# Kernel optimization log

Hardware: AMD Instinct MI355X
Metric: run time of the kernel (lower is better)

Reference implementation:

```python
import jax, jax.numpy as jnp
import numpy as np

HIDDEN = 1000
DICT = 4811
T = 44
B = 256


def _lstm_cell(x, h, c, W_ih, W_hh, b_ih, b_hh):
    # gates: [B, 4*H], PyTorch order i, f, g, o
    gates = x @ W_ih.T + b_ih + h @ W_hh.T + b_hh
    i, f, g, o = jnp.split(gates, 4, axis=-1)
    i = jax.nn.sigmoid(i)
    f = jax.nn.sigmoid(f)
    g = jnp.tanh(g)
    o = jax.nn.sigmoid(o)
    c_new = f * c + i * g
    h_new = o * jnp.tanh(c_new)
    return h_new, c_new


def setup_inputs() -> dict:
    key = jax.random.key(0)
    ks = jax.random.split(key, 20)
    s = 0.02
    H = HIDDEN
    return {
        "x": jax.random.normal(ks[0], (B, T, H), jnp.float32),
        "h1": jax.random.normal(ks[1], (B, H), jnp.float32),
        "h2": jax.random.normal(ks[2], (B, H), jnp.float32),
        "c1": jax.random.normal(ks[3], (B, H), jnp.float32),
        "c2": jax.random.normal(ks[4], (B, H), jnp.float32),
        "layer_W": jax.random.normal(ks[5], (H, H), jnp.float32) * s,
        "layer_b": jnp.zeros((H,), jnp.float32),
        "W_ih1": jax.random.normal(ks[6], (4 * H, 2 * H), jnp.float32) * s,
        "W_hh1": jax.random.normal(ks[7], (4 * H, H), jnp.float32) * s,
        "b_ih1": jnp.zeros((4 * H,), jnp.float32),
        "b_hh1": jnp.zeros((4 * H,), jnp.float32),
        "W_ih2": jax.random.normal(ks[8], (4 * H, DICT + 2 * H), jnp.float32) * s,
        "W_hh2": jax.random.normal(ks[9], (4 * H, H), jnp.float32) * s,
        "b_ih2": jnp.zeros((4 * H,), jnp.float32),
        "b_hh2": jnp.zeros((4 * H,), jnp.float32),
        "out_W": jax.random.normal(ks[10], (DICT, H), jnp.float32) * s,
        "out_b": jnp.zeros((DICT,), jnp.float32),
    }


def reference(x, h1, h2, c1, c2, layer_W, layer_b,
              W_ih1, W_hh1, b_ih1, b_hh1,
              W_ih2, W_hh2, b_ih2, b_hh2,
              out_W, out_b):
    # input projection: [B, T, H]
    xp = x @ layer_W.T + layer_b
    prev0 = jnp.zeros((x.shape[0], DICT), x.dtype)

    def step(carry, xt):
        h1, c1, h2, c2, prev = carry
        l1_in = jnp.concatenate([xt, h1], axis=1)            # [B, 2H]
        h1n, c1n = _lstm_cell(l1_in, h1, c1, W_ih1, W_hh1, b_ih1, b_hh1)
        l2_in = jnp.concatenate([prev, h2, h1n], axis=1)     # [B, DICT+2H]
        h2n, c2n = _lstm_cell(l2_in, h2, c2, W_ih2, W_hh2, b_ih2, b_hh2)
        logits = h2n @ out_W.T + out_b                       # [B, DICT]
        # NOTE: original torch code softmaxes over dim=0 (batch axis)
        y = jax.nn.softmax(logits, axis=0)
        return (h1n, c1n, h2n, c2n, y), y

    xs = jnp.transpose(xp, (1, 0, 2))                        # [T, B, H]
    _, ys = jax.lax.scan(step, (h1, c1, h2, c2, prev0), xs)
    return jnp.transpose(ys, (1, 0, 2))                      # [B, T, DICT]
```

## Files before the change

kernel.cpp:

```cpp
#include <hip/hip_runtime.h>
#include <hip/hip_bf16.h>

#define HID   1000
#define DICT  4811
#define TT    44
#define BB    256
#define G4    4000
#define G4P   4096
#define K1P   2048
#define K2P   6912
#define HP    1024
#define DP    4864
#define Z2_H2 4864
#define Z2_H1 5888
#define PD    3
#define GPART ((long long)BB * G4P)

typedef __attribute__((ext_vector_type(8))) short short8;
typedef __attribute__((ext_vector_type(4))) float f32x4;

__device__ __forceinline__ short f2b(float f) {
    unsigned u = __float_as_uint(f);
    unsigned r = (u + 0x7FFFu + ((u >> 16) & 1u)) >> 16;
    return (short)r;
}

__device__ __forceinline__ void gload16(const void* g, const short* l) {
    __builtin_amdgcn_global_load_lds(
        (const __attribute__((address_space(1))) unsigned int*)g,
        (__attribute__((address_space(3))) unsigned int*)l, 16, 0, 0);
}

__global__ void prep_w1p(const float* __restrict__ wih1, const float* __restrict__ whh1,
                         short* __restrict__ w) {
    for (size_t i = (size_t)blockIdx.x * blockDim.x + threadIdx.x; i < (size_t)G4P * K1P;
         i += (size_t)gridDim.x * blockDim.x) {
        int n = (int)(i >> 11), j = (int)(i & 2047);
        float v = 0.f;
        if (n < G4) {
            if (j < HID) v = wih1[(size_t)n * 2000 + j];
            else if (j >= 1024 && j < 1024 + HID) {
                int jj = j - 1024;
                v = wih1[(size_t)n * 2000 + HID + jj] + whh1[(size_t)n * HID + jj];
            }
        }
        w[i] = f2b(v);
    }
}

__global__ void prep_w2p(const float* __restrict__ wih2, const float* __restrict__ whh2,
                         short* __restrict__ w) {
    int n = blockIdx.y;
    int j = blockIdx.x * 256 + threadIdx.x;
    float v = 0.f;
    if (n < G4) {
        if (j < DICT) v = wih2[(size_t)n * 6811 + j];
        else if (j >= Z2_H2 && j < Z2_H2 + HID) {
            int jj = j - Z2_H2;
            v = wih2[(size_t)n * 6811 + DICT + jj] + whh2[(size_t)n * HID + jj];
        } else if (j >= Z2_H1 && j < Z2_H1 + HID) {
            int jj = j - Z2_H1;
            v = wih2[(size_t)n * 6811 + DICT + HID + jj];
        }
    }
    w[(size_t)n * K2P + j] = f2b(v);
}

__global__ void prep_outwp(const float* __restrict__ outw, short* __restrict__ w) {
    int n = blockIdx.y;
    int j = blockIdx.x * 256 + threadIdx.x;
    float v = (n < DICT && j < HID) ? outw[(size_t)n * HID + j] : 0.f;
    w[(size_t)n * HP + j] = f2b(v);
}

__global__ void prep_cvt(const float* __restrict__ src, short* __restrict__ dst, size_t n) {
    for (size_t i = (size_t)blockIdx.x * blockDim.x + threadIdx.x; i < n;
         i += (size_t)gridDim.x * blockDim.x)
        dst[i] = f2b(src[i]);
}

__global__ void prep_addv(const float* __restrict__ a, const float* __restrict__ b,
                          float* __restrict__ dst, int n) {
    int i = blockIdx.x * blockDim.x + threadIdx.x;
    if (i < n) dst[i] = a[i] + b[i];
}

__global__ void init_vec(const float* __restrict__ src, short* __restrict__ dst, int ld) {
    int i = blockIdx.x * blockDim.x + threadIdx.x;
    if (i >= BB * HID) return;
    int b = i / HID, h = i % HID;
    dst[(size_t)b * ld + h] = f2b(src[i]);
}

template <int EPI, int AF32>
__global__ __launch_bounds__(256) void gemm_nt(
    const void* __restrict__ Ap, int lda,
    const short* __restrict__ Bp, int ldb,
    const float* __restrict__ bias,
    void* __restrict__ Cp, long long partStride, int ldc,
    int M, int N, int Kvalid)
{
    __shared__ short As[64][40];
    __shared__ short Bs[64][40];
    const int tid  = threadIdx.x;
    const int lane = tid & 63;
    const int wave = tid >> 6;
    const int wm = wave >> 1, wn = wave & 1;
    const int tm = blockIdx.y * 64, tn = blockIdx.x * 64;
    const int srow = tid >> 2;
    const int scol = (tid & 3) * 8;

    const int nk = (Kvalid + 31) >> 5;
    const int s0 = (int)(((long long)nk * blockIdx.z) / gridDim.z);
    const int s1 = (int)(((long long)nk * (blockIdx.z + 1)) / gridDim.z);

    const int arow = tm + srow;
    const int brow = tn + srow;
    const bool bvalid = brow < N;

    auto loadA = [&](int ks) -> short8 {
        int k = (ks << 5) + scol;
        short8 r = {0, 0, 0, 0, 0, 0, 0, 0};
        if (k + 8 <= Kvalid) {
            if (AF32) {
                const f32x4* p = (const f32x4*)((const float*)Ap + (size_t)arow * lda + k);
                f32x4 u0 = p[0], u1 = p[1];
                r[0] = f2b(u0[0]); r[1] = f2b(u0[1]); r[2] = f2b(u0[2]); r[3] = f2b(u0[3]);
                r[4] = f2b(u1[0]); r[5] = f2b(u1[1]); r[6] = f2b(u1[2]); r[7] = f2b(u1[3]);
            } else {
                r = *(const short8*)((const short*)Ap + (size_t)arow * lda + k);
            }
        }
        return r;
    };
    auto loadB = [&](int ks) -> short8 {
        int k = (ks << 5) + scol;
        short8 r = {0, 0, 0, 0, 0, 0, 0, 0};
        if (bvalid && (k + 8 <= Kvalid))
            r = *(const short8*)(Bp + (size_t)brow * ldb + k);
        return r;
    };

    f32x4 acc[2][2];
    for (int a = 0; a < 2; ++a)
        for (int b = 0; b < 2; ++b)
            acc[a][b] = (f32x4){0.f, 0.f, 0.f, 0.f};

    short8 ra = loadA(s0), rb = loadB(s0);
    *(short8*)&As[srow][scol] = ra;
    *(short8*)&Bs[srow][scol] = rb;
    __syncthreads();

    const int kg = (lane >> 4) * 8;
    const int fr = lane & 15;

    for (int s = s0; s < s1; ++s) {
        short8 a0 = *(short8*)&As[wm * 32 + fr][kg];
        short8 a1 = *(short8*)&As[wm * 32 + 16 + fr][kg];
        short8 b0 = *(short8*)&Bs[wn * 32 + fr][kg];
        short8 b1 = *(short8*)&Bs[wn * 32 + 16 + fr][kg];
        short8 na, nb;
        if (s + 1 < s1) { na = loadA(s + 1); nb = loadB(s + 1); }
        acc[0][0] = __builtin_amdgcn_mfma_f32_16x16x32_bf16(a0, b0, acc[0][0], 0, 0, 0);
        acc[0][1] = __builtin_amdgcn_mfma_f32_16x16x32_bf16(a0, b1, acc[0][1], 0, 0, 0);
        acc[1][0] = __builtin_amdgcn_mfma_f32_16x16x32_bf16(a1, b0, acc[1][0], 0, 0, 0);
        acc[1][1] = __builtin_amdgcn_mfma_f32_16x16x32_bf16(a1, b1, acc[1][1], 0, 0, 0);
        __syncthreads();
        if (s + 1 < s1) {
            *(short8*)&As[srow][scol] = na;
            *(short8*)&Bs[srow][scol] = nb;
        }
        __syncthreads();
    }

    float* Cf = (float*)Cp + (size_t)partStride * blockIdx.z;
    for (int mi = 0; mi < 2; ++mi)
        for (int ni = 0; ni < 2; ++ni) {
            int col = tn + wn * 32 + ni * 16 + (lane & 15);
            if (col >= N) continue;
            float bv = bias ? bias[col] : 0.f;
            int row0 = tm + wm * 32 + mi * 16 + ((lane >> 4) << 2);
            f32x4 v = acc[mi][ni];
            for (int j = 0; j < 4; ++j) {
                int row = row0 + j;
                float val = v[j] + bv;
                if (EPI == 0) {
                    Cf[(size_t)row * ldc + col] = val;
                } else {
                    int b = row / TT, t = row % TT;
                    ((short*)Cp)[((size_t)t * BB + b) * ldc + col] = f2b(val);
                }
            }
        }
}

__global__ __launch_bounds__(512, 4) void gemm_s128(
    const short* __restrict__ A0, const short* __restrict__ A1, int splitA, int lda,
    const short* __restrict__ Bw, int ldb,
    float* __restrict__ C, long long partStride, int ldc, int nk)
{
    __shared__ __align__(16) short smem[PD][8192];
    const int tid  = threadIdx.x;
    const int lane = tid & 63;
    const int w    = tid >> 6;
    const int wm = w >> 2, wn = w & 3;
    const int tm = blockIdx.y * 128;
    const int tn = blockIdx.x * 128;
    const int s0 = (int)(((long long)nk * blockIdx.z) / gridDim.z);
    const int s1 = (int)(((long long)nk * (blockIdx.z + 1)) / gridDim.z);

    const int rA = tid >> 2, slA = tid & 3;
    const int swz = (slA ^ ((rA >> 1) & 3)) << 3;
    const size_t aoff = (size_t)(tm + rA) * lda + (size_t)swz;
    const size_t boff = (size_t)(tn + rA) * ldb + (size_t)swz;

    auto stage = [&](int buf, int s) {
        const int k0 = s << 5;
        const short* As = (k0 < splitA) ? A0 : A1;
        const short* l = &smem[buf][0];
        gload16(As + k0 + aoff, l + tid * 8);
        gload16(Bw + k0 + boff, l + 4096 + tid * 8);
    };

    const int fr = lane & 15;
    const int kg = lane >> 4;
    int aRd[4], bRd[2];
    #pragma unroll
    for (int mi = 0; mi < 4; ++mi) {
        int row = wm * 64 + mi * 16 + fr;
        aRd[mi] = row * 32 + ((kg ^ ((row >> 1) & 3)) << 3);
    }
    #pragma unroll
    for (int ni = 0; ni < 2; ++ni) {
        int row = wn * 32 + ni * 16 + fr;
        bRd[ni] = 4096 + row * 32 + ((kg ^ ((row >> 1) & 3)) << 3);
    }

    f32x4 acc[4][2];
    #pragma unroll
    for (int a = 0; a < 4; ++a)
        #pragma unroll
        for (int b = 0; b < 2; ++b)
            acc[a][b] = (f32x4){0.f, 0.f, 0.f, 0.f};

    #pragma unroll
    for (int i = 0; i < PD; ++i)
        if (s0 + i < s1) stage(i, s0 + i);

    int buf = 0;
    for (int s = s0; s < s1; ++s) {
        const int ahead = s1 - 1 - s;
        if (ahead >= 2)      asm volatile("s_waitcnt vmcnt(4)" ::: "memory");
        else if (ahead == 1) asm volatile("s_waitcnt vmcnt(2)" ::: "memory");
        else                 asm volatile("s_waitcnt vmcnt(0)" ::: "memory");
        __builtin_amdgcn_s_barrier();

        const short* bp = &smem[buf][0];
        short8 af[4], bf[2];
        #pragma unroll
        for (int i = 0; i < 4; ++i) af[i] = *(const short8*)(bp + aRd[i]);
        #pragma unroll
        for (int i = 0; i < 2; ++i) bf[i] = *(const short8*)(bp + bRd[i]);
        asm volatile("s_waitcnt lgkmcnt(0)" ::: "memory");
        __builtin_amdgcn_sched_barrier(0);
        __builtin_amdgcn_s_barrier();
        if (s + PD < s1) stage(buf, s + PD);

        #pragma unroll
        for (int mi = 0; mi < 4; ++mi)
            #pragma unroll
            for (int ni = 0; ni < 2; ++ni)
                acc[mi][ni] = __builtin_amdgcn_mfma_f32_16x16x32_bf16(af[mi], bf[ni], acc[mi][ni], 0, 0, 0);

        buf = (buf + 1 == PD) ? 0 : buf + 1;
    }

    float* Cp = C + (size_t)partStride * blockIdx.z;
    const int colb = tn + wn * 32 + fr;
    const int rowb = tm + wm * 64 + (kg << 2);
    #pragma unroll
    for (int mi = 0; mi < 4; ++mi)
        #pragma unroll
        for (int ni = 0; ni < 2; ++ni) {
            int col = colb + ni * 16;
            int row0 = rowb + mi * 16;
            #pragma unroll
            for (int j = 0; j < 4; ++j)
                Cp[(size_t)(row0 + j) * ldc + col] = acc[mi][ni][j];
        }
}

__global__ __launch_bounds__(512) void logits_sm(
    const short* __restrict__ A , const short* __restrict__ Bw ,
    const float* __restrict__ outb, float* __restrict__ out,
    short* __restrict__ z2, int t)
{
    __shared__ __align__(16) short smem[PD][10240];
    __shared__ float red[256];
    const int tid  = threadIdx.x;
    const int lane = tid & 63;
    const int w    = tid >> 6;
    const int wm = w >> 1, wn = w & 1;
    const int tn = blockIdx.x * 64;
    const int nk = HP / 32;

    const int cA0 = w * 64 + lane;
    const int cA1 = cA0 + 512;
    const int rA0 = cA0 >> 2, rA1 = cA1 >> 2;
    const size_t aoff0 = (size_t)rA0 * HP + (size_t)((((cA0 & 3) ^ ((rA0 >> 1) & 3))) << 3);
    const size_t aoff1 = (size_t)rA1 * HP + (size_t)((((cA1 & 3) ^ ((rA1 >> 1) & 3))) << 3);
    const int cB = w * 32 + (lane & 31);
    const int rB = cB >> 2;
    const size_t boff = (size_t)(tn + rB) * HP + (size_t)((((cB & 3) ^ ((rB >> 1) & 3))) << 3);

    auto stage = [&](int buf, int s) {
        const int k0 = s << 5;
        const short* l = &smem[buf][0];
        gload16(A + k0 + aoff0, l + w * 512);
        gload16(A + k0 + aoff1, l + 4096 + w * 512);
        if (lane < 32) gload16(Bw + k0 + boff, l + 8192 + w * 256);
    };

    const int fr = lane & 15;
    const int kg = lane >> 4;
    int aRd[4], bRd[2];
    #pragma unroll
    for (int mi = 0; mi < 4; ++mi) {
        int row = wm * 64 + mi * 16 + fr;
        aRd[mi] = row * 32 + ((kg ^ ((row >> 1) & 3)) << 3);
    }
    #pragma unroll
    for (int ni = 0; ni < 2; ++ni) {
        int row = wn * 32 + ni * 16 + fr;
        bRd[ni] = 8192 + row * 32 + ((kg ^ ((row >> 1) & 3)) << 3);
    }

    f32x4 acc[4][2];
    #pragma unroll
    for (int a = 0; a < 4; ++a)
        #pragma unroll
        for (int b = 0; b < 2; ++b)
            acc[a][b] = (f32x4){0.f, 0.f, 0.f, 0.f};

    #pragma unroll
    for (int i = 0; i < PD; ++i) stage(i, i);

    int buf = 0;
    for (int s = 0; s < nk; ++s) {
        const int ahead = nk - 1 - s;
        if (ahead >= 2)      asm volatile("s_waitcnt vmcnt(6)" ::: "memory");
        else if (ahead == 1) asm volatile("s_waitcnt vmcnt(3)" ::: "memory");
        else                 asm volatile("s_waitcnt vmcnt(0)" ::: "memory");
        __builtin_amdgcn_s_barrier();

        const short* bp = &smem[buf][0];
        short8 af[4], bf[2];
        #pragma unroll
        for (int i = 0; i < 4; ++i) af[i] = *(const short8*)(bp + aRd[i]);
        #pragma unroll
        for (int i = 0; i < 2; ++i) bf[i] = *(const short8*)(bp + bRd[i]);
        asm volatile("s_waitcnt lgkmcnt(0)" ::: "memory");
        __builtin_amdgcn_sched_barrier(0);
        __builtin_amdgcn_s_barrier();
        if (s + PD < nk) stage(buf, s + PD);

        #pragma unroll
        for (int mi = 0; mi < 4; ++mi)
            #pragma unroll
            for (int ni = 0; ni < 2; ++ni)
                acc[mi][ni] = __builtin_amdgcn_mfma_f32_16x16x32_bf16(af[mi], bf[ni], acc[mi][ni], 0, 0, 0);

        buf = (buf + 1 == PD) ? 0 : buf + 1;
    }

    int   colv[2];
    float bv[2];
    #pragma unroll
    for (int ni = 0; ni < 2; ++ni) {
        colv[ni] = tn + wn * 32 + ni * 16 + fr;
        bv[ni] = (colv[ni] < DICT) ? outb[colv[ni]] : 0.f;
    }
    float v[4][2][4];
    float mx[2] = {-3e38f, -3e38f};
    #pragma unroll
    for (int mi = 0; mi < 4; ++mi)
        #pragma unroll
        for (int ni = 0; ni < 2; ++ni)
            #pragma unroll
            for (int j = 0; j < 4; ++j) {
                float x = acc[mi][ni][j] + bv[ni];
                v[mi][ni][j] = x;
                mx[ni] = fmaxf(mx[ni], x);
            }
    #pragma unroll
    for (int ni = 0; ni < 2; ++ni) {
        mx[ni] = fmaxf(mx[ni], __shfl_xor(mx[ni], 16));
        mx[ni] = fmaxf(mx[ni], __shfl_xor(mx[ni], 32));
    }
    if (lane < 16) {
        red[wm * 64 + wn * 32 + fr]      = mx[0];
        red[wm * 64 + wn * 32 + 16 + fr] = mx[1];
    }
    __syncthreads();
    float m[2];
    #pragma unroll
    for (int ni = 0; ni < 2; ++ni) {
        int c = wn * 32 + ni * 16 + fr;
        m[ni] = fmaxf(fmaxf(red[c], red[64 + c]), fmaxf(red[128 + c], red[192 + c]));
    }
    __syncthreads();
    float s2[2] = {0.f, 0.f};
    #pragma unroll
    for (int mi = 0; mi < 4; ++mi)
        #pragma unroll
        for (int ni = 0; ni < 2; ++ni)
            #pragma unroll
            for (int j = 0; j < 4; ++j) {
                float e = expf(v[mi][ni][j] - m[ni]);
                v[mi][ni][j] = e;
                s2[ni] += e;
            }
    #pragma unroll
    for (int ni = 0; ni < 2; ++ni) {
        s2[ni] += __shfl_xor(s2[ni], 16);
        s2[ni] += __shfl_xor(s2[ni], 32);
    }
    if (lane < 16) {
        red[wm * 64 + wn * 32 + fr]      = s2[0];
        red[wm * 64 + wn * 32 + 16 + fr] = s2[1];
    }
    __syncthreads();
    float inv[2];
    #pragma unroll
    for (int ni = 0; ni < 2; ++ni) {
        int c = wn * 32 + ni * 16 + fr;
        inv[ni] = 1.f / (red[c] + red[64 + c] + red[128 + c] + red[192 + c]);
    }
    const int rowb = wm * 64 + (kg << 2);
    #pragma unroll
    for (int mi = 0; mi < 4; ++mi)
        #pragma unroll
        for (int j = 0; j < 4; ++j) {
            int b = rowb + mi * 16 + j;
            #pragma unroll
            for (int ni = 0; ni < 2; ++ni) {
                if (colv[ni] < DICT) {
                    float y = v[mi][ni][j] * inv[ni];
                    out[(size_t)b * ((size_t)TT * DICT) + (size_t)t * DICT + colv[ni]] = y;
                    z2[(size_t)b * K2P + colv[ni]] = f2b(y);
                }
            }
        }
}

template <int NP>
__global__ void lstm_ewN(const float* __restrict__ g, long long ps,
                         const float* __restrict__ bias, float* __restrict__ c,
                         short* __restrict__ d1, int ld1,
                         short* __restrict__ d2, int ld2)
{
    int i = blockIdx.x * blockDim.x + threadIdx.x;
    if (i >= BB * HID) return;
    int b = i / HID, h = i % HID;
    size_t base = (size_t)b * G4P + h;
    float gi = bias[h], gf = bias[HID + h], gg = bias[2 * HID + h], go = bias[3 * HID + h];
    #pragma unroll
    for (int p = 0; p < NP; ++p) {
        const float* gp = g + (size_t)ps * p + base;
        gi += gp[0];
        gf += gp[HID];
        gg += gp[2 * HID];
        go += gp[3 * HID];
    }
    float ii = 1.f / (1.f + expf(-gi));
    float ff = 1.f / (1.f + expf(-gf));
    float tg = tanhf(gg);
    float oo = 1.f / (1.f + expf(-go));
    float cn = ff * c[i] + ii * tg;
    c[i] = cn;
    float hn = oo * tanhf(cn);
    short hb = f2b(hn);
    d1[(size_t)b * ld1 + h] = hb;
    d2[(size_t)b * ld2 + h] = hb;
}

extern "C" void kernel_launch(void* const* d_in, const int* in_sizes, int n_in,
                              void* d_out, int out_size, void* d_ws, size_t ws_size,
                              hipStream_t stream)
{
    const float* x    = (const float*)d_in[0];
    const float* h1   = (const float*)d_in[1];
    const float* h2   = (const float*)d_in[2];
    const float* c1in = (const float*)d_in[3];
    const float* c2in = (const float*)d_in[4];
    const float* layW = (const float*)d_in[5];
    const float* layb = (const float*)d_in[6];
    const float* Wih1 = (const float*)d_in[7];
    const float* Whh1 = (const float*)d_in[8];
    const float* bih1 = (const float*)d_in[9];
    const float* bhh1 = (const float*)d_in[10];
    const float* Wih2 = (const float*)d_in[11];
    const float* Whh2 = (const float*)d_in[12];
    const float* bih2 = (const float*)d_in[13];
    const float* bhh2 = (const float*)d_in[14];
    const float* outW = (const float*)d_in[15];
    const float* outb = (const float*)d_in[16];
    float* out = (float*)d_out;
    (void)in_sizes; (void)n_in; (void)out_size; (void)ws_size;

    char* ws = (char*)d_ws;
    size_t off = 0;
    auto alloc = [&](size_t bytes) -> void* {
        size_t p = off;
        off = (off + bytes + 255) & ~(size_t)255;
        return (void*)(ws + p);
    };

    short* w1cat = (short*)alloc((size_t)G4P * K1P * 2);
    short* w2cat = (short*)alloc((size_t)G4P * K2P * 2);
    short* outwb = (short*)alloc((size_t)DP * HP * 2);
    short* laywb = (short*)alloc((size_t)HID * HID * 2);
    short* xp    = (short*)alloc((size_t)TT * BB * HP * 2);
    short* h1pad = (short*)alloc((size_t)BB * HP * 2);
    short* h2pad = (short*)alloc((size_t)BB * HP * 2);
    short* z2    = (short*)alloc((size_t)BB * K2P * 2);
    float* gbuf  = (float*)alloc((size_t)8 * BB * G4P * 4);
    float* c1    = (float*)alloc((size_t)BB * HID * 4);
    float* c2    = (float*)alloc((size_t)BB * HID * 4);
    float* bias1 = (float*)alloc((size_t)G4 * 4);
    float* bias2 = (float*)alloc((size_t)G4 * 4);

    hipMemsetAsync(xp, 0, (size_t)TT * BB * HP * 2, stream);
    hipMemsetAsync(z2, 0, (size_t)BB * K2P * 2, stream);
    hipMemsetAsync(h1pad, 0, (size_t)BB * HP * 2, stream);
    hipMemsetAsync(h2pad, 0, (size_t)BB * HP * 2, stream);

    prep_w1p<<<4096, 256, 0, stream>>>(Wih1, Whh1, w1cat);
    prep_w2p<<<dim3(27, G4P), 256, 0, stream>>>(Wih2, Whh2, w2cat);
    prep_outwp<<<dim3(4, DP), 256, 0, stream>>>(outW, outwb);
    prep_cvt<<<1024, 256, 0, stream>>>(layW, laywb, (size_t)HID * HID);
    prep_addv<<<16, 256, 0, stream>>>(bih1, bhh1, bias1, G4);
    prep_addv<<<16, 256, 0, stream>>>(bih2, bhh2, bias2, G4);
    init_vec<<<1000, 256, 0, stream>>>(h1, h1pad, HP);
    init_vec<<<1000, 256, 0, stream>>>(h2, h2pad, HP);
    init_vec<<<1000, 256, 0, stream>>>(h2, z2 + Z2_H2, K2P);
    hipMemcpyAsync(c1, c1in, (size_t)BB * HID * 4, hipMemcpyDeviceToDevice, stream);
    hipMemcpyAsync(c2, c2in, (size_t)BB * HID * 4, hipMemcpyDeviceToDevice, stream);

    gemm_nt<1, 1><<<dim3(16, (BB * TT) / 64, 1), 256, 0, stream>>>(
        x, HID, laywb, HID, layb, xp, 0, HP, BB * TT, HID, HID);

    for (int t = 0; t < TT; ++t) {
        gemm_s128<<<dim3(32, 2, 4), 512, 0, stream>>>(
            xp + (size_t)t * BB * HP, h1pad - HP, 1024, HP, w1cat, K1P, gbuf, GPART, G4P, K1P / 32);
        lstm_ewN<4><<<1000, 256, 0, stream>>>(gbuf, GPART, bias1, c1, z2 + Z2_H1, K2P, h1pad, HP);

        gemm_s128<<<dim3(32, 2, 8), 512, 0, stream>>>(
            z2, z2, 0, K2P, w2cat, K2P, gbuf, GPART, G4P, K2P / 32);
        lstm_ewN<8><<<1000, 256, 0, stream>>>(gbuf, GPART, bias2, c2, z2 + Z2_H2, K2P, h2pad, HP);

        logits_sm<<<76, 512, 0, stream>>>(h2pad, outwb, outb, out, z2, t);
    }
}
```

Baseline: 3.428 ms.

## Fuse LSTM elementwise into split-K gate GEMM via last-block reduction

Interleaves gate weight rows (i,f,g,o per hidden unit) so each GEMM tile holds all four gates of 32 hidden units. The last split-K block for a tile, found with an atomic counter, sums the partials, applies bias and the LSTM nonlinearities, and writes c and h. This removes the separate elementwise launches. Double-buffered h1 and z2 buffers avoid read/write hazards between the in-place updates and concurrent readers. The cost is a serialized tail reduction done by a few blocks, plus extra fences and atomics.

```diff
diff --git a/kernel.cpp b/kernel.cpp
--- a/kernel.cpp
+++ b/kernel.cpp
@@ -5,12 +5,10 @@
 #define DICT  4811
 #define TT    44
 #define BB    256
-#define G4    4000
 #define G4P   4096
 #define K1P   2048
 #define K2P   6912
 #define HP    1024
-#define DP    4864
 #define Z2_H2 4864
 #define Z2_H1 5888
 #define PD    3
@@ -31,36 +29,40 @@
         (__attribute__((address_space(3))) unsigned int*)l, 16, 0, 0);
 }
 
-__global__ void prep_w1p(const float* __restrict__ wih1, const float* __restrict__ whh1,
+__global__ void prep_w1i(const float* __restrict__ wih1, const float* __restrict__ whh1,
                          short* __restrict__ w) {
     for (size_t i = (size_t)blockIdx.x * blockDim.x + threadIdx.x; i < (size_t)G4P * K1P;
          i += (size_t)gridDim.x * blockDim.x) {
         int n = (int)(i >> 11), j = (int)(i & 2047);
+        int h = n >> 2, g = n & 3;
         float v = 0.f;
-        if (n < G4) {
-            if (j < HID) v = wih1[(size_t)n * 2000 + j];
+        if (h < HID) {
+            int r = g * HID + h;
+            if (j < HID) v = wih1[(size_t)r * 2000 + j];
             else if (j >= 1024 && j < 1024 + HID) {
                 int jj = j - 1024;
-                v = wih1[(size_t)n * 2000 + HID + jj] + whh1[(size_t)n * HID + jj];
+                v = wih1[(size_t)r * 2000 + HID + jj] + whh1[(size_t)r * HID + jj];
             }
         }
         w[i] = f2b(v);
     }
 }
 
-__global__ void prep_w2p(const float* __restrict__ wih2, const float* __restrict__ whh2,
+__global__ void prep_w2i(const float* __restrict__ wih2, const float* __restrict__ whh2,
                          short* __restrict__ w) {
     int n = blockIdx.y;
     int j = blockIdx.x * 256 + threadIdx.x;
+    int h = n >> 2, g = n & 3;
     float v = 0.f;
-    if (n < G4) {
-        if (j < DICT) v = wih2[(size_t)n * 6811 + j];
+    if (h < HID) {
+        int r = g * HID + h;
+        if (j < DICT) v = wih2[(size_t)r * 6811 + j];
         else if (j >= Z2_H2 && j < Z2_H2 + HID) {
             int jj = j - Z2_H2;
-            v = wih2[(size_t)n * 6811 + DICT + jj] + whh2[(size_t)n * HID + jj];
+            v = wih2[(size_t)r * 6811 + DICT + jj] + whh2[(size_t)r * HID + jj];
         } else if (j >= Z2_H1 && j < Z2_H1 + HID) {
             int jj = j - Z2_H1;
-            v = wih2[(size_t)n * 6811 + DICT + HID + jj];
+            v = wih2[(size_t)r * 6811 + DICT + HID + jj];
         }
     }
     w[(size_t)n * K2P + j] = f2b(v);
@@ -79,10 +81,12 @@
         dst[i] = f2b(src[i]);
 }
 
-__global__ void prep_addv(const float* __restrict__ a, const float* __restrict__ b,
-                          float* __restrict__ dst, int n) {
-    int i = blockIdx.x * blockDim.x + threadIdx.x;
-    if (i < n) dst[i] = a[i] + b[i];
+__global__ void prep_biasi(const float* __restrict__ bi, const float* __restrict__ bh,
+                           float* __restrict__ dst) {
+    int n = blockIdx.x * 256 + threadIdx.x;
+    if (n >= 4096) return;
+    int h = n >> 2, g = n & 3;
+    dst[n] = (h < HID) ? bi[g * HID + h] + bh[g * HID + h] : 0.f;
 }
 
 __global__ void init_vec(const float* __restrict__ src, short* __restrict__ dst, int ld) {
@@ -194,12 +198,17 @@
         }
 }
 
-__global__ __launch_bounds__(512, 4) void gemm_s128(
+template <int SPLIT>
+__global__ __launch_bounds__(512, 4) void gatesF(
     const short* __restrict__ A0, const short* __restrict__ A1, int splitA, int lda,
     const short* __restrict__ Bw, int ldb,
-    float* __restrict__ C, long long partStride, int ldc, int nk)
+    float* __restrict__ gbuf, int nk,
+    const f32x4* __restrict__ bias4, float* __restrict__ c,
+    short* __restrict__ d1, int ld1, short* __restrict__ d2, int ld2,
+    int* __restrict__ cnt)
 {
     __shared__ __align__(16) short smem[PD][8192];
+    __shared__ int lastFlag;
     const int tid  = threadIdx.x;
     const int lane = tid & 63;
     const int w    = tid >> 6;
@@ -275,7 +284,7 @@
         buf = (buf + 1 == PD) ? 0 : buf + 1;
     }
 
-    float* Cp = C + (size_t)partStride * blockIdx.z;
+    float* Cp = gbuf + (size_t)GPART * blockIdx.z;
     const int colb = tn + wn * 32 + fr;
     const int rowb = tm + wm * 64 + (kg << 2);
     #pragma unroll
@@ -286,8 +295,43 @@
             int row0 = rowb + mi * 16;
             #pragma unroll
             for (int j = 0; j < 4; ++j)
-                Cp[(size_t)(row0 + j) * ldc + col] = acc[mi][ni][j];
-        }
+                Cp[(size_t)(row0 + j) * G4P + col] = acc[mi][ni][j];
+        }
+
+    __syncthreads();
+    __threadfence();
+    const int tile = blockIdx.y * 32 + blockIdx.x;
+    if (tid == 0)
+        lastFlag = (atomicAdd(&cnt[tile], 1) == SPLIT - 1) ? 1 : 0;
+    __syncthreads();
+    if (!lastFlag) return;
+    __threadfence();
+
+    const int b_loc = tid & 127;
+    const int hq = tid >> 7;
+    const int bg = blockIdx.y * 128 + b_loc;
+    const size_t crow = (size_t)bg * HID;
+    #pragma unroll
+    for (int j = 0; j < 8; ++j) {
+        int h_loc = hq * 8 + j;
+        int h_g = blockIdx.x * 32 + h_loc;
+        if (h_g >= HID) continue;
+        size_t n4 = (size_t)blockIdx.x * 128 + h_loc * 4;
+        f32x4 g4 = bias4[h_g];
+        #pragma unroll
+        for (int p = 0; p < SPLIT; ++p)
+            g4 += *(const f32x4*)(gbuf + (size_t)GPART * p + (size_t)bg * G4P + n4);
+        float ii = 1.f / (1.f + expf(-g4[0]));
+        float ff = 1.f / (1.f + expf(-g4[1]));
+        float tg = tanhf(g4[2]);
+        float oo = 1.f / (1.f + expf(-g4[3]));
+        float cn = ff * c[crow + h_g] + ii * tg;
+        c[crow + h_g] = cn;
+        short hb = f2b(oo * tanhf(cn));
+        d1[(size_t)bg * ld1 + h_g] = hb;
+        d2[(size_t)bg * ld2 + h_g] = hb;
+    }
+    if (tid == 0) cnt[tile] = 0;
 }
 
 __global__ __launch_bounds__(512) void logits_sm(
@@ -405,8 +449,8 @@
     float m[2];
     #pragma unroll
     for (int ni = 0; ni < 2; ++ni) {
-        int c = wn * 32 + ni * 16 + fr;
-        m[ni] = fmaxf(fmaxf(red[c], red[64 + c]), fmaxf(red[128 + c], red[192 + c]));
+        int cc = wn * 32 + ni * 16 + fr;
+        m[ni] = fmaxf(fmaxf(red[cc], red[64 + cc]), fmaxf(red[128 + cc], red[192 + cc]));
     }
     __syncthreads();
     float s2[2] = {0.f, 0.f};
@@ -433,8 +477,8 @@
     float inv[2];
     #pragma unroll
     for (int ni = 0; ni < 2; ++ni) {
-        int c = wn * 32 + ni * 16 + fr;
-        inv[ni] = 1.f / (red[c] + red[64 + c] + red[128 + c] + red[192 + c]);
+        int cc = wn * 32 + ni * 16 + fr;
+        inv[ni] = 1.f / (red[cc] + red[64 + cc] + red[128 + cc] + red[192 + cc]);
     }
     const int rowb = wm * 64 + (kg << 2);
     #pragma unroll
@@ -451,37 +495,6 @@
                 }
             }
         }
-}
-
-template <int NP>
-__global__ void lstm_ewN(const float* __restrict__ g, long long ps,
-                         const float* __restrict__ bias, float* __restrict__ c,
-                         short* __restrict__ d1, int ld1,
-                         short* __restrict__ d2, int ld2)
-{
-    int i = blockIdx.x * blockDim.x + threadIdx.x;
-    if (i >= BB * HID) return;
-    int b = i / HID, h = i % HID;
-    size_t base = (size_t)b * G4P + h;
-    float gi = bias[h], gf = bias[HID + h], gg = bias[2 * HID + h], go = bias[3 * HID + h];
-    #pragma unroll
-    for (int p = 0; p < NP; ++p) {
-        const float* gp = g + (size_t)ps * p + base;
-        gi += gp[0];
-        gf += gp[HID];
-        gg += gp[2 * HID];
-        go += gp[3 * HID];
-    }
-    float ii = 1.f / (1.f + expf(-gi));
-    float ff = 1.f / (1.f + expf(-gf));
-    float tg = tanhf(gg);
-    float oo = 1.f / (1.f + expf(-go));
-    float cn = ff * c[i] + ii * tg;
-    c[i] = cn;
-    float hn = oo * tanhf(cn);
-    short hb = f2b(hn);
-    d1[(size_t)b * ld1 + h] = hb;
-    d2[(size_t)b * ld2 + h] = hb;
 }
 
 extern "C" void kernel_launch(void* const* d_in, const int* in_sizes, int n_in,
@@ -516,34 +529,39 @@
         return (void*)(ws + p);
     };
 
-    short* w1cat = (short*)alloc((size_t)G4P * K1P * 2);
-    short* w2cat = (short*)alloc((size_t)G4P * K2P * 2);
-    short* outwb = (short*)alloc((size_t)DP * HP * 2);
+    short* w1i   = (short*)alloc((size_t)G4P * K1P * 2);
+    short* w2i   = (short*)alloc((size_t)G4P * K2P * 2);
+    short* outwb = (short*)alloc((size_t)4864 * HP * 2);
     short* laywb = (short*)alloc((size_t)HID * HID * 2);
     short* xp    = (short*)alloc((size_t)TT * BB * HP * 2);
-    short* h1pad = (short*)alloc((size_t)BB * HP * 2);
+    short* h1A   = (short*)alloc((size_t)BB * HP * 2);
+    short* h1B   = (short*)alloc((size_t)BB * HP * 2);
     short* h2pad = (short*)alloc((size_t)BB * HP * 2);
-    short* z2    = (short*)alloc((size_t)BB * K2P * 2);
+    short* z2a   = (short*)alloc((size_t)BB * K2P * 2);
+    short* z2b   = (short*)alloc((size_t)BB * K2P * 2);
     float* gbuf  = (float*)alloc((size_t)8 * BB * G4P * 4);
     float* c1    = (float*)alloc((size_t)BB * HID * 4);
     float* c2    = (float*)alloc((size_t)BB * HID * 4);
-    float* bias1 = (float*)alloc((size_t)G4 * 4);
-    float* bias2 = (float*)alloc((size_t)G4 * 4);
+    float* bi1   = (float*)alloc((size_t)G4P * 4);
+    float* bi2   = (float*)alloc((size_t)G4P * 4);
+    int*   cnt   = (int*)alloc(64 * 4);
 
     hipMemsetAsync(xp, 0, (size_t)TT * BB * HP * 2, stream);
-    hipMemsetAsync(z2, 0, (size_t)BB * K2P * 2, stream);
-    hipMemsetAsync(h1pad, 0, (size_t)BB * HP * 2, stream);
+    hipMemsetAsync(z2a, 0, (size_t)BB * K2P * 2, stream);
+    hipMemsetAsync(z2b, 0, (size_t)BB * K2P * 2, stream);
+    hipMemsetAsync(h1A, 0, (size_t)BB * HP * 2, stream);
+    hipMemsetAsync(h1B, 0, (size_t)BB * HP * 2, stream);
     hipMemsetAsync(h2pad, 0, (size_t)BB * HP * 2, stream);
-
-    prep_w1p<<<4096, 256, 0, stream>>>(Wih1, Whh1, w1cat);
-    prep_w2p<<<dim3(27, G4P), 256, 0, stream>>>(Wih2, Whh2, w2cat);
-    prep_outwp<<<dim3(4, DP), 256, 0, stream>>>(outW, outwb);
+    hipMemsetAsync(cnt, 0, 64 * 4, stream);
+
+    prep_w1i<<<4096, 256, 0, stream>>>(Wih1, Whh1, w1i);
+    prep_w2i<<<dim3(27, G4P), 256, 0, stream>>>(Wih2, Whh2, w2i);
+    prep_outwp<<<dim3(4, 4864), 256, 0, stream>>>(outW, outwb);
     prep_cvt<<<1024, 256, 0, stream>>>(layW, laywb, (size_t)HID * HID);
-    prep_addv<<<16, 256, 0, stream>>>(bih1, bhh1, bias1, G4);
-    prep_addv<<<16, 256, 0, stream>>>(bih2, bhh2, bias2, G4);
-    init_vec<<<1000, 256, 0, stream>>>(h1, h1pad, HP);
-    init_vec<<<1000, 256, 0, stream>>>(h2, h2pad, HP);
-    init_vec<<<1000, 256, 0, stream>>>(h2, z2 + Z2_H2, K2P);
+    prep_biasi<<<16, 256, 0, stream>>>(bih1, bhh1, bi1);
+    prep_biasi<<<16, 256, 0, stream>>>(bih2, bhh2, bi2);
+    init_vec<<<1000, 256, 0, stream>>>(h1, h1A, HP);
+    init_vec<<<1000, 256, 0, stream>>>(h2, z2a + Z2_H2, K2P);
     hipMemcpyAsync(c1, c1in, (size_t)BB * HID * 4, hipMemcpyDeviceToDevice, stream);
     hipMemcpyAsync(c2, c2in, (size_t)BB * HID * 4, hipMemcpyDeviceToDevice, stream);
 
@@ -551,14 +569,19 @@
         x, HID, laywb, HID, layb, xp, 0, HP, BB * TT, HID, HID);
 
     for (int t = 0; t < TT; ++t) {
-        gemm_s128<<<dim3(32, 2, 4), 512, 0, stream>>>(
-            xp + (size_t)t * BB * HP, h1pad - HP, 1024, HP, w1cat, K1P, gbuf, GPART, G4P, K1P / 32);
-        lstm_ewN<4><<<1000, 256, 0, stream>>>(gbuf, GPART, bias1, c1, z2 + Z2_H1, K2P, h1pad, HP);
-
-        gemm_s128<<<dim3(32, 2, 8), 512, 0, stream>>>(
-            z2, z2, 0, K2P, w2cat, K2P, gbuf, GPART, G4P, K2P / 32);
-        lstm_ewN<8><<<1000, 256, 0, stream>>>(gbuf, GPART, bias2, c2, z2 + Z2_H2, K2P, h2pad, HP);
-
-        logits_sm<<<76, 512, 0, stream>>>(h2pad, outwb, outb, out, z2, t);
-    }
-}
+        short* zin  = (t & 1) ? z2b : z2a;
+        short* zout = (t & 1) ? z2a : z2b;
+        short* hcur = (t & 1) ? h1B : h1A;
+        short* hnxt = (t & 1) ? h1A : h1B;
+
+        gatesF<4><<<dim3(32, 2, 4), 512, 0, stream>>>(
+            xp + (size_t)t * BB * HP, hcur - HP, 1024, HP, w1i, K1P, gbuf, K1P / 32,
+            (const f32x4*)bi1, c1, zin + Z2_H1, K2P, hnxt, HP, cnt);
+
+        gatesF<8><<<dim3(32, 2, 8), 512, 0, stream>>>(
+            zin, zin, 0, K2P, w2i, K2P, gbuf, K2P / 32,
+            (const f32x4*)bi2, c2, zout + Z2_H2, K2P, h2pad, HP, cnt);
+
+        logits_sm<<<76, 512, 0, stream>>>(h2pad, outwb, outb, out, zout, t);
+    }
+}
```

New measurement: 13.55 ms. 3.95x slower.

## Fuse layer-1 LSTM GEMM with gate epilogue using interleaved gate weights

Applied to the files above, without the earlier changes.

Layer 1's weight rows are interleaved so the four gates of each hidden unit sit next to each other. That lets a new 64x64-tile GEMM kernel compute the full K without split-K and apply the LSTM cell update in its epilogue. This removes the split-K partial buffer round trip and one elementwise launch per step. h1 is double-buffered so the fused kernel can write the next state while other blocks still read the current one. Layer 2's split-K is reduced from 8 to 4, which gives fewer partials to sum but less parallelism across blocks.

```diff
diff --git a/kernel.cpp b/kernel.cpp
--- a/kernel.cpp
+++ b/kernel.cpp
@@ -10,7 +10,6 @@
 #define K1P   2048
 #define K2P   6912
 #define HP    1024
-#define DP    4864
 #define Z2_H2 4864
 #define Z2_H1 5888
 #define PD    3
@@ -31,17 +30,19 @@
         (__attribute__((address_space(3))) unsigned int*)l, 16, 0, 0);
 }
 
-__global__ void prep_w1p(const float* __restrict__ wih1, const float* __restrict__ whh1,
+__global__ void prep_w1i(const float* __restrict__ wih1, const float* __restrict__ whh1,
                          short* __restrict__ w) {
     for (size_t i = (size_t)blockIdx.x * blockDim.x + threadIdx.x; i < (size_t)G4P * K1P;
          i += (size_t)gridDim.x * blockDim.x) {
         int n = (int)(i >> 11), j = (int)(i & 2047);
+        int h = n >> 2, g = n & 3;
         float v = 0.f;
-        if (n < G4) {
-            if (j < HID) v = wih1[(size_t)n * 2000 + j];
+        if (h < HID) {
+            int r = g * HID + h;
+            if (j < HID) v = wih1[(size_t)r * 2000 + j];
             else if (j >= 1024 && j < 1024 + HID) {
                 int jj = j - 1024;
-                v = wih1[(size_t)n * 2000 + HID + jj] + whh1[(size_t)n * HID + jj];
+                v = wih1[(size_t)r * 2000 + HID + jj] + whh1[(size_t)r * HID + jj];
             }
         }
         w[i] = f2b(v);
@@ -83,6 +84,14 @@
                           float* __restrict__ dst, int n) {
     int i = blockIdx.x * blockDim.x + threadIdx.x;
     if (i < n) dst[i] = a[i] + b[i];
+}
+
+__global__ void prep_biasi(const float* __restrict__ bi, const float* __restrict__ bh,
+                           float* __restrict__ dst) {
+    int n = blockIdx.x * 256 + threadIdx.x;
+    if (n >= 4096) return;
+    int h = n >> 2, g = n & 3;
+    dst[n] = (h < HID) ? bi[g * HID + h] + bh[g * HID + h] : 0.f;
 }
 
 __global__ void init_vec(const float* __restrict__ src, short* __restrict__ dst, int ld) {
@@ -194,6 +203,123 @@
         }
 }
 
+__global__ __launch_bounds__(256) void gates1F(
+    const short* __restrict__ xp_t,
+    const short* __restrict__ h1m,
+    const short* __restrict__ w1i,
+    const f32x4* __restrict__ bias4,
+    float* __restrict__ c1,
+    short* __restrict__ zh1,
+    short* __restrict__ h1nxt)
+{
+    __shared__ __align__(16) short smem[PD][4096];
+    const int tid  = threadIdx.x;
+    const int lane = tid & 63;
+    const int w    = tid >> 6;
+    const int wm = w >> 1, wn = w & 1;
+    const int tm = blockIdx.y * 64;
+    const int tn = blockIdx.x * 64;
+    const int nk = K1P / 32;
+
+    const int rA = tid >> 2, sl = tid & 3;
+    const int swz = (sl ^ ((rA >> 1) & 3)) << 3;
+    const size_t aoff = (size_t)(tm + rA) * HP + (size_t)swz;
+    const size_t boff = (size_t)(tn + rA) * K1P + (size_t)swz;
+
+    auto stage = [&](int buf, int s) {
+        const int k0 = s << 5;
+        const short* As = (k0 < 1024) ? xp_t : h1m;
+        const short* l = &smem[buf][0];
+        gload16(As + k0 + aoff, l + tid * 8);
+        gload16(w1i + k0 + boff, l + 2048 + tid * 8);
+    };
+
+    const int fr = lane & 15;
+    const int kg = lane >> 4;
+    int aRd[2], bRd[2];
+    #pragma unroll
+    for (int mi = 0; mi < 2; ++mi) {
+        int row = wm * 32 + mi * 16 + fr;
+        aRd[mi] = row * 32 + ((kg ^ ((row >> 1) & 3)) << 3);
+    }
+    #pragma unroll
+    for (int ni = 0; ni < 2; ++ni) {
+        int row = wn * 32 + ni * 16 + fr;
+        bRd[ni] = 2048 + row * 32 + ((kg ^ ((row >> 1) & 3)) << 3);
+    }
+
+    f32x4 acc[2][2];
+    #pragma unroll
+    for (int a = 0; a < 2; ++a)
+        #pragma unroll
+        for (int b = 0; b < 2; ++b)
+            acc[a][b] = (f32x4){0.f, 0.f, 0.f, 0.f};
+
+    #pragma unroll
+    for (int i = 0; i < PD; ++i) stage(i, i);
+
+    int buf = 0;
+    for (int s = 0; s < nk; ++s) {
+        const int ahead = nk - 1 - s;
+        if (ahead >= 2)      asm volatile("s_waitcnt vmcnt(4)" ::: "memory");
+        else if (ahead == 1) asm volatile("s_waitcnt vmcnt(2)" ::: "memory");
+        else                 asm volatile("s_waitcnt vmcnt(0)" ::: "memory");
+        __builtin_amdgcn_s_barrier();
+
+        const short* bp = &smem[buf][0];
+        short8 af[2], bf[2];
+        #pragma unroll
+        for (int i = 0; i < 2; ++i) af[i] = *(const short8*)(bp + aRd[i]);
+        #pragma unroll
+        for (int i = 0; i < 2; ++i) bf[i] = *(const short8*)(bp + bRd[i]);
+        asm volatile("s_waitcnt lgkmcnt(0)" ::: "memory");
+        __builtin_amdgcn_sched_barrier(0);
+        __builtin_amdgcn_s_barrier();
+        if (s + PD < nk) stage(buf, s + PD);
+
+        #pragma unroll
+        for (int mi = 0; mi < 2; ++mi)
+            #pragma unroll
+            for (int ni = 0; ni < 2; ++ni)
+                acc[mi][ni] = __builtin_amdgcn_mfma_f32_16x16x32_bf16(af[mi], bf[ni], acc[mi][ni], 0, 0, 0);
+
+        buf = (buf + 1 == PD) ? 0 : buf + 1;
+    }
+
+    float* gl = (float*)&smem[0][0];
+    #pragma unroll
+    for (int mi = 0; mi < 2; ++mi)
+        #pragma unroll
+        for (int ni = 0; ni < 2; ++ni) {
+            int row = wm * 32 + mi * 16 + kg * 4;
+            int col = wn * 32 + ni * 16 + fr;
+            #pragma unroll
+            for (int j = 0; j < 4; ++j)
+                gl[(row + j) * 68 + col] = acc[mi][ni][j];
+        }
+    __syncthreads();
+
+    const int b_loc = tid & 63;
+    const int b_g = tm + b_loc;
+    #pragma unroll
+    for (int q = 0; q < 4; ++q) {
+        int h_loc = (tid >> 6) * 4 + q;
+        int h_g = blockIdx.x * 16 + h_loc;
+        if (h_g >= HID) continue;
+        f32x4 g4 = *(const f32x4*)(gl + b_loc * 68 + h_loc * 4);
+        g4 += bias4[h_g];
+        float ii = 1.f / (1.f + expf(-g4[0]));
+        float ff = 1.f / (1.f + expf(-g4[1]));
+        float tg = tanhf(g4[2]);
+        float oo = 1.f / (1.f + expf(-g4[3]));
+        float cn = ff * c1[(size_t)b_g * HID + h_g] + ii * tg;
+        c1[(size_t)b_g * HID + h_g] = cn;
+        short hb = f2b(oo * tanhf(cn));
+        zh1[(size_t)b_g * K2P + h_g] = hb;
+        h1nxt[(size_t)b_g * HP + h_g] = hb;
+    }
+}
+
 __global__ __launch_bounds__(512, 4) void gemm_s128(
     const short* __restrict__ A0, const short* __restrict__ A1, int splitA, int lda,
     const short* __restrict__ Bw, int ldb,
@@ -405,8 +531,8 @@
     float m[2];
     #pragma unroll
     for (int ni = 0; ni < 2; ++ni) {
-        int c = wn * 32 + ni * 16 + fr;
-        m[ni] = fmaxf(fmaxf(red[c], red[64 + c]), fmaxf(red[128 + c], red[192 + c]));
+        int cc = wn * 32 + ni * 16 + fr;
+        m[ni] = fmaxf(fmaxf(red[cc], red[64 + cc]), fmaxf(red[128 + cc], red[192 + cc]));
     }
     __syncthreads();
     float s2[2] = {0.f, 0.f};
@@ -433,8 +559,8 @@
     float inv[2];
     #pragma unroll
     for (int ni = 0; ni < 2; ++ni) {
-        int c = wn * 32 + ni * 16 + fr;
-        inv[ni] = 1.f / (red[c] + red[64 + c] + red[128 + c] + red[192 + c]);
+        int cc = wn * 32 + ni * 16 + fr;
+        inv[ni] = 1.f / (red[cc] + red[64 + cc] + red[128 + cc] + red[192 + cc]);
     }
     const int rowb = wm * 64 + (kg << 2);
     #pragma unroll
@@ -516,32 +642,34 @@
         return (void*)(ws + p);
     };
 
-    short* w1cat = (short*)alloc((size_t)G4P * K1P * 2);
+    short* w1i   = (short*)alloc((size_t)G4P * K1P * 2);
     short* w2cat = (short*)alloc((size_t)G4P * K2P * 2);
-    short* outwb = (short*)alloc((size_t)DP * HP * 2);
+    short* outwb = (short*)alloc((size_t)4864 * HP * 2);
     short* laywb = (short*)alloc((size_t)HID * HID * 2);
     short* xp    = (short*)alloc((size_t)TT * BB * HP * 2);
-    short* h1pad = (short*)alloc((size_t)BB * HP * 2);
+    short* h1A   = (short*)alloc((size_t)BB * HP * 2);
+    short* h1B   = (short*)alloc((size_t)BB * HP * 2);
     short* h2pad = (short*)alloc((size_t)BB * HP * 2);
     short* z2    = (short*)alloc((size_t)BB * K2P * 2);
-    float* gbuf  = (float*)alloc((size_t)8 * BB * G4P * 4);
+    float* gbuf  = (float*)alloc((size_t)4 * BB * G4P * 4);
     float* c1    = (float*)alloc((size_t)BB * HID * 4);
     float* c2    = (float*)alloc((size_t)BB * HID * 4);
-    float* bias1 = (float*)alloc((size_t)G4 * 4);
+    float* bi1   = (float*)alloc((size_t)G4P * 4);
     float* bias2 = (float*)alloc((size_t)G4 * 4);
 
     hipMemsetAsync(xp, 0, (size_t)TT * BB * HP * 2, stream);
     hipMemsetAsync(z2, 0, (size_t)BB * K2P * 2, stream);
-    hipMemsetAsync(h1pad, 0, (size_t)BB * HP * 2, stream);
+    hipMemsetAsync(h1A, 0, (size_t)BB * HP * 2, stream);
+    hipMemsetAsync(h1B, 0, (size_t)BB * HP * 2, stream);
     hipMemsetAsync(h2pad, 0, (size_t)BB * HP * 2, stream);
 
-    prep_w1p<<<4096, 256, 0, stream>>>(Wih1, Whh1, w1cat);
+    prep_w1i<<<4096, 256, 0, stream>>>(Wih1, Whh1, w1i);
     prep_w2p<<<dim3(27, G4P), 256, 0, stream>>>(Wih2, Whh2, w2cat);
-    prep_outwp<<<dim3(4, DP), 256, 0, stream>>>(outW, outwb);
+    prep_outwp<<<dim3(4, 4864), 256, 0, stream>>>(outW, outwb);
     prep_cvt<<<1024, 256, 0, stream>>>(layW, laywb, (size_t)HID * HID);
-    prep_addv<<<16, 256, 0, stream>>>(bih1, bhh1, bias1, G4);
+    prep_biasi<<<16, 256, 0, stream>>>(bih1, bhh1, bi1);
     prep_addv<<<16, 256, 0, stream>>>(bih2, bhh2, bias2, G4);
-    init_vec<<<1000, 256, 0, stream>>>(h1, h1pad, HP);
+    init_vec<<<1000, 256, 0, stream>>>(h1, h1A, HP);
     init_vec<<<1000, 256, 0, stream>>>(h2, h2pad, HP);
     init_vec<<<1000, 256, 0, stream>>>(h2, z2 + Z2_H2, K2P);
     hipMemcpyAsync(c1, c1in, (size_t)BB * HID * 4, hipMemcpyDeviceToDevice, stream);
@@ -551,13 +679,17 @@
         x, HID, laywb, HID, layb, xp, 0, HP, BB * TT, HID, HID);
 
     for (int t = 0; t < TT; ++t) {
+        short* hcur = (t & 1) ? h1B : h1A;
+        short* hnxt = (t & 1) ? h1A : h1B;
+
+        gates1F<<<dim3(64, 4), 256, 0, stream>>>(
+            xp + (size_t)t * BB * HP, hcur - HP, w1i,
+            (const f32x4*)bi1, c1, z2 + Z2_H1, hnxt);
+
         gemm_s128<<<dim3(32, 2, 4), 512, 0, stream>>>(
-            xp + (size_t)t * BB * HP, h1pad - HP, 1024, HP, w1cat, K1P, gbuf, GPART, G4P, K1P / 32);
-        lstm_ewN<4><<<1000, 256, 0, stream>>>(gbuf, GPART, bias1, c1, z2 + Z2_H1, K2P, h1pad, HP);
-
-        gemm_s128<<<dim3(32, 2, 8), 512, 0, stream>>>(
             z2, z2, 0, K2P, w2cat, K2P, gbuf, GPART, G4P, K2P / 32);
-        lstm_ewN<8><<<1000, 256, 0, stream>>>(gbuf, GPART, bias2, c2, z2 + Z2_H2, K2P, h2pad, HP);
+        lstm_ewN<4><<<1000, 256, 0, stream>>>(
+            gbuf, GPART, bias2, c2, z2 + Z2_H2, K2P, h2pad, HP);
 
         logits_sm<<<76, 512, 0, stream>>>(h2pad, outwb, outb, out, z2, t);
     }
```

Measured after the change: 3.541 ms. 1.03x slower.
